# Kernel optimization log

Measured on AMD Instinct MI355X. Metric: run time of the kernel, lower is better.

## Reference

```python
import jax, jax.numpy as jnp
import numpy as np

SIZE = 1024
CODE_DIM = 256
B, H, W = 32, 32, 32


def setup_inputs() -> dict:
    key = jax.random.key(0)
    k1, k2 = jax.random.split(key)
    z = jax.random.normal(k1, (B, CODE_DIM, H, W), dtype=jnp.float32)
    embeddings = jax.random.normal(k2, (SIZE, CODE_DIM), dtype=jnp.float32)
    return {"z": z, "embeddings": embeddings}


def reference(z, embeddings):
    b, c, h, w = z.shape  # c == code_dim
    # (b, h, w, c) -> (N, c)
    flat = jnp.transpose(z, (0, 2, 3, 1)).reshape(-1, c)
    d = (
        jnp.sum(flat * flat, axis=-1, keepdims=True)
        - 2.0 * (flat @ embeddings.T)
        + jnp.sum(embeddings * embeddings, axis=-1)
    )
    idx = jnp.argmin(d, axis=-1)  # (N,)
    quantized = embeddings[idx].reshape(b, h, w, c)
    quantized = jnp.transpose(quantized, (0, 3, 1, 2))  # (b, c, h, w)
    straight_through = jax.lax.stop_gradient(quantized - z) + z
    return quantized, straight_through, idx.reshape(b, h, w)
```

## Files before the change

kernel.cpp:

```cpp
#include <hip/hip_runtime.h>

#define NPTS   32768
#define NCODES 1024
#define DIM    256
#define HWSZ   1024
#define CHW    (DIM*HWSZ)
#define QSZ    8388608

typedef __attribute__((ext_vector_type(8))) short short8;
typedef __attribute__((ext_vector_type(4))) float f32x4;

__device__ __forceinline__ void gload16(const void* g, void* l) {
    __builtin_amdgcn_global_load_lds((const __attribute__((address_space(1))) void*)g,
                                     (__attribute__((address_space(3))) void*)l,
                                     16, 0, 0);
}

__device__ __forceinline__ unsigned bf16_rne(float f) {
    unsigned u = __float_as_uint(f);
    return (u + 0x7fffu + ((u >> 16) & 1u)) >> 16;
}

__global__ void k_prep_e(const float* __restrict__ emb, short* __restrict__ Eh,
                         short* __restrict__ El, float* __restrict__ e2) {
    int tid = threadIdx.x, lane = tid & 63, w = tid >> 6;
    int k = blockIdx.x * 4 + w;
    const float4 v = *reinterpret_cast<const float4*>(emb + k * DIM + lane * 4);
    float f[4] = {v.x, v.y, v.z, v.w};
    short h[4], l[4];
    double s = 0.0;
    #pragma unroll
    for (int i = 0; i < 4; ++i) {
        unsigned hb = bf16_rne(f[i]);
        float hf = __uint_as_float(hb << 16);
        h[i] = (short)hb;
        l[i] = (short)bf16_rne(f[i] - hf);
        s += (double)f[i] * f[i];
    }
    *reinterpret_cast<short4*>(Eh + k * DIM + lane * 4) = make_short4(h[0], h[1], h[2], h[3]);
    *reinterpret_cast<short4*>(El + k * DIM + lane * 4) = make_short4(l[0], l[1], l[2], l[3]);
    #pragma unroll
    for (int m = 32; m >= 1; m >>= 1) s += __shfl_xor(s, m);
    if (lane == 0) e2[k] = (float)s;
}

__global__ void k_prep_x(const float* __restrict__ z, short* __restrict__ Xh,
                         short* __restrict__ Xl) {
    __shared__ float T[64][65];
    int blk = blockIdx.x;
    int b   = blk >> 6;
    int ct  = (blk >> 4) & 3;
    int ht  = blk & 15;
    int c0 = ct * 64, hw0 = ht * 64;
    int tid = threadIdx.x;
    int cc = tid & 63, r0 = tid >> 6;
    const float* zp = z + b * CHW;
    #pragma unroll
    for (int i = 0; i < 16; ++i) {
        int r = r0 + i * 4;
        T[r][cc] = zp[(c0 + r) * HWSZ + hw0 + cc];
    }
    __syncthreads();
    int cl = tid & 63;
    #pragma unroll
    for (int i = 0; i < 16; ++i) {
        int hwl = r0 + i * 4;
        float f = T[cl][hwl];
        unsigned hb = bf16_rne(f);
        float hf = __uint_as_float(hb << 16);
        unsigned lb = bf16_rne(f - hf);
        int n = b * HWSZ + hw0 + hwl;
        Xh[n * DIM + c0 + cl] = (short)hb;
        Xl[n * DIM + c0 + cl] = (short)lb;
    }
}

__launch_bounds__(256, 3)
__global__ void k_dist(const short* __restrict__ Xh, const short* __restrict__ Xl,
                       const short* __restrict__ Eh, const short* __restrict__ El,
                       const float* __restrict__ e2, float* __restrict__ minv,
                       int* __restrict__ mini) {
    __shared__ __align__(16) short Ah[4096];
    __shared__ __align__(16) short Al[4096];
    __shared__ __align__(16) short Bh[4096];
    __shared__ __align__(16) short Bl[4096];
    __shared__ float sv[2][128];
    __shared__ int   si[2][128];

    const int tid = threadIdx.x;
    const int pt = blockIdx.x & 255;
    const int ct = blockIdx.x >> 8;
    const int n0 = pt * 128;
    const int c0 = ct * 128;

    const int w = tid >> 6, lane = tid & 63;
    const int wr = w >> 1, wc = w & 1;
    const int m16 = lane & 15, quad = lane >> 4;

    f32x4 acc[4][4];
    #pragma unroll
    for (int i = 0; i < 4; ++i)
        #pragma unroll
        for (int j = 0; j < 4; ++j) acc[i][j] = (f32x4){0.f, 0.f, 0.f, 0.f};

    const int r  = lane >> 2;
    const int ks = (lane & 3) * 8;
    const int ldsoff0 = (w * 16) * 64;
    const int ldsoff1 = (64 + w * 16) * 64;
    const int arow0 = (n0 + w * 16 + r) * DIM;
    const int arow1 = (n0 + 64 + w * 16 + r) * DIM;
    const int brow0 = (c0 + w * 16 + r) * DIM;
    const int brow1 = (c0 + 64 + w * 16 + r) * DIM;

    for (int t = 0; t < 8; ++t) {
        const int koff = t * 32 + ks;
        __syncthreads();
        gload16(Xh + arow0 + koff, (char*)Ah + ldsoff0);
        gload16(Xh + arow1 + koff, (char*)Ah + ldsoff1);
        gload16(Xl + arow0 + koff, (char*)Al + ldsoff0);
        gload16(Xl + arow1 + koff, (char*)Al + ldsoff1);
        gload16(Eh + brow0 + koff, (char*)Bh + ldsoff0);
        gload16(Eh + brow1 + koff, (char*)Bh + ldsoff1);
        gload16(El + brow0 + koff, (char*)Bl + ldsoff0);
        gload16(El + brow1 + koff, (char*)Bl + ldsoff1);
        __syncthreads();

        short8 ah[4], al[4], bh[4], bl[4];
        #pragma unroll
        for (int i = 0; i < 4; ++i) {
            int ar = (wr * 64 + i * 16 + m16) * 32 + quad * 8;
            ah[i] = *(const short8*)&Ah[ar];
            al[i] = *(const short8*)&Al[ar];
        }
        #pragma unroll
        for (int j = 0; j < 4; ++j) {
            int br = (wc * 64 + j * 16 + m16) * 32 + quad * 8;
            bh[j] = *(const short8*)&Bh[br];
            bl[j] = *(const short8*)&Bl[br];
        }
        #pragma unroll
        for (int i = 0; i < 4; ++i)
            #pragma unroll
            for (int j = 0; j < 4; ++j)
                acc[i][j] = __builtin_amdgcn_mfma_f32_16x16x32_bf16(ah[i], bh[j], acc[i][j], 0, 0, 0);
        #pragma unroll
        for (int i = 0; i < 4; ++i)
            #pragma unroll
            for (int j = 0; j < 4; ++j)
                acc[i][j] = __builtin_amdgcn_mfma_f32_16x16x32_bf16(al[i], bh[j], acc[i][j], 0, 0, 0);
        #pragma unroll
        for (int i = 0; i < 4; ++i)
            #pragma unroll
            for (int j = 0; j < 4; ++j)
                acc[i][j] = __builtin_amdgcn_mfma_f32_16x16x32_bf16(ah[i], bl[j], acc[i][j], 0, 0, 0);
    }

    float ecol[4];
    #pragma unroll
    for (int j = 0; j < 4; ++j) ecol[j] = e2[c0 + wc * 64 + j * 16 + m16];

    #pragma unroll
    for (int i = 0; i < 4; ++i) {
        #pragma unroll
        for (int rr = 0; rr < 4; ++rr) {
            float best = 3.4e38f; int bi = 0;
            #pragma unroll
            for (int j = 0; j < 4; ++j) {
                float d = fmaf(-2.f, acc[i][j][rr], ecol[j]);
                int code = c0 + wc * 64 + j * 16 + m16;
                if (d < best) { best = d; bi = code; }
            }
            #pragma unroll
            for (int m = 1; m < 16; m <<= 1) {
                float ov = __shfl_xor(best, m);
                int   oi = __shfl_xor(bi, m);
                if (ov < best || (ov == best && oi < bi)) { best = ov; bi = oi; }
            }
            if (m16 == 0) {
                int p = wr * 64 + i * 16 + quad * 4 + rr;
                sv[wc][p] = best; si[wc][p] = bi;
            }
        }
    }
    __syncthreads();
    if (tid < 128) {
        float v0 = sv[0][tid]; int i0 = si[0][tid];
        float v1 = sv[1][tid]; int i1 = si[1][tid];
        if (v1 < v0) { v0 = v1; i0 = i1; }
        minv[ct * NPTS + n0 + tid] = v0;
        mini[ct * NPTS + n0 + tid] = i0;
    }
}

__global__ void k_out(const float* __restrict__ z, const float* __restrict__ emb,
                      const float* __restrict__ minv, const int* __restrict__ mini,
                      float* __restrict__ out) {
    __shared__ int sbi[64];
    int n0 = blockIdx.x * 64;
    int tid = threadIdx.x;
    if (tid < 64) {
        int n = n0 + tid;
        float bv = minv[n]; int bi = mini[n];
        #pragma unroll
        for (int g = 1; g < 8; ++g) {
            float v = minv[g * NPTS + n]; int ii = mini[g * NPTS + n];
            if (v < bv) { bv = v; bi = ii; }
        }
        sbi[tid] = bi;
        out[2 * QSZ + n] = (float)bi;
    }
    __syncthreads();
    int hwq = tid & 15, cb = tid >> 4;
    int b = n0 >> 10, hw0 = (n0 & 1023) + hwq * 4;
    const float* ep0 = emb + sbi[hwq * 4 + 0] * DIM;
    const float* ep1 = emb + sbi[hwq * 4 + 1] * DIM;
    const float* ep2 = emb + sbi[hwq * 4 + 2] * DIM;
    const float* ep3 = emb + sbi[hwq * 4 + 3] * DIM;
    #pragma unroll 4
    for (int c = cb; c < DIM; c += 16) {
        int off = b * CHW + c * HWSZ + hw0;
        float4 zv = *reinterpret_cast<const float4*>(z + off);
        float4 q = make_float4(ep0[c], ep1[c], ep2[c], ep3[c]);
        *reinterpret_cast<float4*>(out + off) = q;
        float4 st = make_float4((q.x - zv.x) + zv.x, (q.y - zv.y) + zv.y,
                                (q.z - zv.z) + zv.z, (q.w - zv.w) + zv.w);
        *reinterpret_cast<float4*>(out + QSZ + off) = st;
    }
}

extern "C" void kernel_launch(void* const* d_in, const int* in_sizes, int n_in,
                              void* d_out, int out_size, void* d_ws, size_t ws_size,
                              hipStream_t stream) {
    const float* z   = (const float*)d_in[0];
    const float* emb = (const float*)d_in[1];
    float* out = (float*)d_out;
    float* ws  = (float*)d_ws;

    short* Eh   = (short*)ws;
    short* El   = (short*)(ws + 131072);
    float* e2   = ws + 262144;
    float* minv = ws + 263168;
    int*   mini = (int*)(ws + 525312);

    short* Xh = (short*)out;
    short* Xl = (short*)(out + 4194304);

    hipLaunchKernelGGL(k_prep_e, dim3(256),  dim3(256), 0, stream, emb, Eh, El, e2);
    hipLaunchKernelGGL(k_prep_x, dim3(2048), dim3(256), 0, stream, z, Xh, Xl);
    hipLaunchKernelGGL(k_dist,   dim3(2048), dim3(256), 0, stream, Xh, Xl, Eh, El, e2, minv, mini);
    hipLaunchKernelGGL(k_out,    dim3(512),  dim3(256), 0, stream, z, emb, minv, mini, out);
}
```

Baseline: 190.4 us.

## Vectorize prep_x transpose stores, stage codebook rows in LDS for output, raise dist occupancy

k_prep_x now handles 32 spatial points across all channels per block. It reads z with float4 loads and writes each point's bf16 hi/lo halves as 16-byte short8 vectors instead of scalar shorts. k_out first gathers the 32 selected codebook rows into a padded LDS tile with float4 loads, then builds the transposed output from LDS instead of issuing strided scalar global gathers. The k_dist launch bound is raised to 4 blocks per CU, which may force register spills.

```diff
diff --git a/kernel.cpp b/kernel.cpp
--- a/kernel.cpp
+++ b/kernel.cpp
@@ -46,36 +46,43 @@
 
 __global__ void k_prep_x(const float* __restrict__ z, short* __restrict__ Xh,
                          short* __restrict__ Xl) {
-    __shared__ float T[64][65];
+    __shared__ float T[64][33];
     int blk = blockIdx.x;
-    int b   = blk >> 6;
-    int ct  = (blk >> 4) & 3;
-    int ht  = blk & 15;
-    int c0 = ct * 64, hw0 = ht * 64;
+    int b  = blk >> 5;
+    int ht = blk & 31;
+    int hw0 = ht * 32;
+    int n0  = b * HWSZ + hw0;
     int tid = threadIdx.x;
-    int cc = tid & 63, r0 = tid >> 6;
+    int hq = tid & 7, cr = tid >> 3;
+    int wp = tid >> 3, wc = tid & 7;
     const float* zp = z + b * CHW;
     #pragma unroll
-    for (int i = 0; i < 16; ++i) {
-        int r = r0 + i * 4;
-        T[r][cc] = zp[(c0 + r) * HWSZ + hw0 + cc];
-    }
-    __syncthreads();
-    int cl = tid & 63;
-    #pragma unroll
-    for (int i = 0; i < 16; ++i) {
-        int hwl = r0 + i * 4;
-        float f = T[cl][hwl];
-        unsigned hb = bf16_rne(f);
-        float hf = __uint_as_float(hb << 16);
-        unsigned lb = bf16_rne(f - hf);
-        int n = b * HWSZ + hw0 + hwl;
-        Xh[n * DIM + c0 + cl] = (short)hb;
-        Xl[n * DIM + c0 + cl] = (short)lb;
-    }
-}
-
-__launch_bounds__(256, 3)
+    for (int cc = 0; cc < 4; ++cc) {
+        int c0 = cc * 64;
+        if (cc) __syncthreads();
+        #pragma unroll
+        for (int p = 0; p < 2; ++p) {
+            int c = p * 32 + cr;
+            float4 v = *reinterpret_cast<const float4*>(zp + (c0 + c) * HWSZ + hw0 + hq * 4);
+            T[c][hq * 4 + 0] = v.x; T[c][hq * 4 + 1] = v.y;
+            T[c][hq * 4 + 2] = v.z; T[c][hq * 4 + 3] = v.w;
+        }
+        __syncthreads();
+        short8 hv, lv;
+        #pragma unroll
+        for (int k = 0; k < 8; ++k) {
+            float f = T[wc * 8 + k][wp];
+            unsigned hb = bf16_rne(f);
+            float hf = __uint_as_float(hb << 16);
+            hv[k] = (short)hb;
+            lv[k] = (short)bf16_rne(f - hf);
+        }
+        *reinterpret_cast<short8*>(Xh + (n0 + wp) * DIM + c0 + wc * 8) = hv;
+        *reinterpret_cast<short8*>(Xl + (n0 + wp) * DIM + c0 + wc * 8) = lv;
+    }
+}
+
+__launch_bounds__(256, 4)
 __global__ void k_dist(const short* __restrict__ Xh, const short* __restrict__ Xl,
                        const short* __restrict__ Eh, const short* __restrict__ El,
                        const float* __restrict__ e2, float* __restrict__ minv,
@@ -195,10 +202,11 @@
 __global__ void k_out(const float* __restrict__ z, const float* __restrict__ emb,
                       const float* __restrict__ minv, const int* __restrict__ mini,
                       float* __restrict__ out) {
-    __shared__ int sbi[64];
-    int n0 = blockIdx.x * 64;
+    __shared__ float Q[32][257];
+    __shared__ int sbi[32];
+    int n0 = blockIdx.x * 32;
     int tid = threadIdx.x;
-    if (tid < 64) {
+    if (tid < 32) {
         int n = n0 + tid;
         float bv = minv[n]; int bi = mini[n];
         #pragma unroll
@@ -210,17 +218,26 @@
         out[2 * QSZ + n] = (float)bi;
     }
     __syncthreads();
-    int hwq = tid & 15, cb = tid >> 4;
-    int b = n0 >> 10, hw0 = (n0 & 1023) + hwq * 4;
-    const float* ep0 = emb + sbi[hwq * 4 + 0] * DIM;
-    const float* ep1 = emb + sbi[hwq * 4 + 1] * DIM;
-    const float* ep2 = emb + sbi[hwq * 4 + 2] * DIM;
-    const float* ep3 = emb + sbi[hwq * 4 + 3] * DIM;
-    #pragma unroll 4
-    for (int c = cb; c < DIM; c += 16) {
+    {
+        int pt = tid >> 3, co = tid & 7;
+        const float* ep = emb + sbi[pt] * DIM;
+        #pragma unroll
+        for (int j = 0; j < 8; ++j) {
+            int c = j * 32 + co * 4;
+            float4 v = *reinterpret_cast<const float4*>(ep + c);
+            Q[pt][c] = v.x; Q[pt][c + 1] = v.y; Q[pt][c + 2] = v.z; Q[pt][c + 3] = v.w;
+        }
+    }
+    __syncthreads();
+    int hq = tid & 7, cr = tid >> 3;
+    int b = n0 >> 10, hw0 = (n0 & 1023) + hq * 4;
+    #pragma unroll
+    for (int it = 0; it < 8; ++it) {
+        int c = it * 32 + cr;
         int off = b * CHW + c * HWSZ + hw0;
         float4 zv = *reinterpret_cast<const float4*>(z + off);
-        float4 q = make_float4(ep0[c], ep1[c], ep2[c], ep3[c]);
+        float4 q = make_float4(Q[hq * 4 + 0][c], Q[hq * 4 + 1][c],
+                               Q[hq * 4 + 2][c], Q[hq * 4 + 3][c]);
         *reinterpret_cast<float4*>(out + off) = q;
         float4 st = make_float4((q.x - zv.x) + zv.x, (q.y - zv.y) + zv.y,
                                 (q.z - zv.z) + zv.z, (q.w - zv.w) + zv.w);
@@ -246,7 +263,7 @@
     short* Xl = (short*)(out + 4194304);
 
     hipLaunchKernelGGL(k_prep_e, dim3(256),  dim3(256), 0, stream, emb, Eh, El, e2);
-    hipLaunchKernelGGL(k_prep_x, dim3(2048), dim3(256), 0, stream, z, Xh, Xl);
+    hipLaunchKernelGGL(k_prep_x, dim3(1024), dim3(256), 0, stream, z, Xh, Xl);
     hipLaunchKernelGGL(k_dist,   dim3(2048), dim3(256), 0, stream, Xh, Xl, Eh, El, e2, minv, mini);
-    hipLaunchKernelGGL(k_out,    dim3(512),  dim3(256), 0, stream, z, emb, minv, mini, out);
-}
+    hipLaunchKernelGGL(k_out,    dim3(1024), dim3(256), 0, stream, z, emb, minv, mini, out);
+}
```

New measurement: 167.9 us. -11.8%, faster.
